# Kernel optimization log

Measured on AMD Instinct MI355X. Metric: run time of the kernel, lower is better.

Reference implementation:

```python
import jax, jax.numpy as jnp
import numpy as np

AXIS = 4  # axis_neuron


def silu(x):
    return x * jax.nn.sigmoid(x)


def setup_inputs() -> dict:
    key = jax.random.key(0)
    ks = jax.random.split(key, 20)
    nf, nloc, nall, nnei, a_sel = 1, 1024, 1024, 64, 20
    n_dim, e_dim, a_dim = 128, 64, 64
    f32 = jnp.float32

    def W(k, i, o):
        return jax.random.normal(k, (i, o), f32) / np.float32(np.sqrt(i))

    angle_in = a_dim + n_dim + 2 * e_dim  # angle_dim with a_compress_rate=0, a_mess_has_n=True
    return {
        "node_ebd_ext": jax.random.normal(ks[0], (nf, nall, n_dim), f32),
        "edge_ebd": jax.random.normal(ks[1], (nf, nloc, nnei, e_dim), f32),
        "h2": jax.random.normal(ks[2], (nf, nloc, nnei, 3), f32),
        "angle_ebd": jax.random.normal(ks[3], (nf, nloc, a_sel, a_sel, a_dim), f32),
        "sw": jax.random.uniform(ks[4], (nf, nloc, nnei), f32),
        "a_sw": jax.random.uniform(ks[5], (nf, nloc, a_sel), f32),
        "W_self": W(ks[6], n_dim, n_dim), "b_self": jnp.zeros((n_dim,), f32),
        "W_sym": W(ks[7], (e_dim + n_dim) * AXIS, n_dim), "b_sym": jnp.zeros((n_dim,), f32),
        "W_ne": W(ks[8], 2 * n_dim + e_dim, n_dim), "b_ne": jnp.zeros((n_dim,), f32),
        "W_es": W(ks[9], 2 * n_dim + e_dim, e_dim), "b_es": jnp.zeros((e_dim,), f32),
        "W_ea1": W(ks[10], angle_in, e_dim), "b_ea1": jnp.zeros((e_dim,), f32),
        "W_ea2": W(ks[11], e_dim, e_dim), "b_ea2": jnp.zeros((e_dim,), f32),
        "W_as": W(ks[12], angle_in, a_dim), "b_as": jnp.zeros((a_dim,), f32),
        "res_n": jnp.full((3, n_dim), 0.1, f32),
        "res_e": jnp.full((2, e_dim), 0.1, f32),
        "res_a": jnp.full((1, a_dim), 0.1, f32),
        "nlist": jax.random.randint(ks[13], (nf, nloc, nnei), 0, nall),
        "nlist_mask": jnp.ones((nf, nloc, nnei), bool),
        "a_nlist_mask": jnp.ones((nf, nloc, a_sel), bool),
    }


def _forward(node_ebd_ext, edge_ebd, h2, angle_ebd, sw, a_sw,
             W_self, b_self, W_sym, b_sym, W_ne, b_ne, W_es, b_es,
             W_ea1, b_ea1, W_ea2, b_ea2, W_as, b_as, res_n, res_e, res_a,
             nlist, nlist_mask, a_nlist_mask):
    nf, nloc, nnei, e_dim = edge_ebd.shape
    a_sel = angle_ebd.shape[2]
    a_dim = angle_ebd.shape[-1]
    n_dim = node_ebd_ext.shape[-1]
    node_ebd = node_ebd_ext[:, :nloc]  # nf x nloc x n_dim

    sw = jnp.where(nlist_mask, sw, 0.0)          # masked switch
    a_sw = jnp.where(a_nlist_mask, a_sw, 0.0)

    # gather neighbor node embeddings: nf x nloc x nnei x n_dim
    idx = jnp.where(nlist_mask, nlist, 0)
    nei_node = jnp.take_along_axis(
        node_ebd_ext, idx.reshape(nf, nloc * nnei)[..., None], axis=1
    ).reshape(nf, nloc, nnei, n_dim)

    # node self mlp
    n_self = silu(node_ebd @ W_self + b_self)

    # symmetrization op: hg = h^T g / nnei; grrg = hg[:axis]^T hg / 3
    def grrg(g):
        gw = g * sw[..., None]
        hg = jnp.einsum('flnt,flnd->fltd', h2, gw) / nnei       # f l 3 d
        out = jnp.einsum('flta,fltd->flad', hg[..., :AXIS], hg) / 3.0
        return out.reshape(nf, nloc, -1)                        # f l (axis*d)

    node_sym = silu(jnp.concatenate([grrg(edge_ebd), grrg(nei_node)], axis=-1) @ W_sym + b_sym)

    # node-edge message: linear over concat([node_i, node_j, edge]) = sum of blocks
    W0, W1, W2 = W_ne[:n_dim], W_ne[n_dim:2 * n_dim], W_ne[2 * n_dim:]
    pre_ne = (node_ebd @ W0)[:, :, None, :] + nei_node @ W1 + edge_ebd @ W2 + b_ne
    n_edge = jnp.sum(silu(pre_ne) * sw[..., None], axis=-2) / nnei

    node_new = node_ebd + res_n[0] * n_self + res_n[1] * node_sym + res_n[2] * n_edge

    # edge self message (same edge_info)
    V0, V1, V2 = W_es[:n_dim], W_es[n_dim:2 * n_dim], W_es[2 * n_dim:]
    edge_self = silu((node_ebd @ V0)[:, :, None, :] + nei_node @ V1 + edge_ebd @ V2 + b_es)

    # ---- angle path ----
    e_ang = jnp.where(a_nlist_mask[..., None], edge_ebd[:, :, :a_sel], 0.0)  # f l a e
    s0, s1, s2 = a_dim, a_dim + n_dim, a_dim + n_dim + e_dim
    A0, A1, A2, A3 = W_ea1[:s0], W_ea1[s0:s1], W_ea1[s1:s2], W_ea1[s2:]
    # angle_info @ W_ea1 without materializing the concat (blocks broadcast)
    pre_ang = (angle_ebd @ A0
               + (node_ebd @ A1)[:, :, None, None, :]
               + (e_ang @ A2)[:, :, None, :, :]   # edge_for_angle_i varies along axis 3
               + (e_ang @ A3)[:, :, :, None, :]   # edge_for_angle_j varies along axis 2
               + b_ea1)
    e_ang_upd = silu(pre_ang)                                     # f l a a e
    weighted = a_sw[:, :, :, None, None] * a_sw[:, :, None, :, None] * e_ang_upd
    reduced = jnp.sum(weighted, axis=-2) / np.float32(np.sqrt(a_sel))  # f l a e
    padded = jnp.pad(reduced, ((0, 0), (0, 0), (0, nnei - a_sel), (0, 0)))
    e_angle_msg = silu(padded @ W_ea2 + b_ea2)
    edge_new = edge_ebd + res_e[0] * edge_self + res_e[1] * e_angle_msg

    # angle self update (same angle_info)
    B0, B1, B2, B3 = W_as[:s0], W_as[s0:s1], W_as[s1:s2], W_as[s2:]
    angle_self = silu(angle_ebd @ B0
                      + (node_ebd @ B1)[:, :, None, None, :]
                      + (e_ang @ B2)[:, :, None, :, :]
                      + (e_ang @ B3)[:, :, :, None, :]
                      + b_as)
    angle_new = angle_ebd + res_a[0] * angle_self
    return node_new, edge_new, angle_new


def reference(node_ebd_ext, edge_ebd, h2, angle_ebd, sw, a_sw,
              W_self, b_self, W_sym, b_sym, W_ne, b_ne, W_es, b_es,
              W_ea1, b_ea1, W_ea2, b_ea2, W_as, b_as, res_n, res_e, res_a,
              nlist, nlist_mask, a_nlist_mask):
    return _forward(node_ebd_ext, edge_ebd, h2, angle_ebd, sw, a_sw,
                    W_self, b_self, W_sym, b_sym, W_ne, b_ne, W_es, b_es,
                    W_ea1, b_ea1, W_ea2, b_ea2, W_as, b_as, res_n, res_e, res_a,
                    nlist, nlist_mask, a_nlist_mask)
```

## Files before the change

### kernel.cpp

```cpp
#include <hip/hip_runtime.h>

#define DEVINL __device__ __forceinline__

#define NLOC 1024
#define NNEI 64
#define NDIM 128
#define EDIM 64
#define ADIM 64
#define ASEL 20

enum : size_t {
  WS_NSELF = 0,
  WS_NW0   = WS_NSELF + 1024*128,
  WS_NV0   = WS_NW0   + 1024*128,
  WS_NA1   = WS_NV0   + 1024*64,
  WS_NB1   = WS_NA1   + 1024*64,
  WS_PA2   = WS_NB1   + 1024*64,
  WS_PA3   = WS_PA2   + 1024*ASEL*64,
  WS_PB2   = WS_PA3   + 1024*ASEL*64,
  WS_PB3   = WS_PB2   + 1024*ASEL*64,
  WS_F32_END = WS_PB3 + 1024*ASEL*64
};
__device__ float g_ws[WS_F32_END];
__device__ float g_red[1024*ASEL*64];

DEVINL float siluf(float x) {
  return x * __builtin_amdgcn_rcpf(1.0f + __expf(-x));
}

__global__ __launch_bounds__(128) void k0_node_pre(
    const float* __restrict__ node,
    const float* __restrict__ W_self, const float* __restrict__ b_self,
    const float* __restrict__ W_ne,   const float* __restrict__ b_ne,
    const float* __restrict__ W_es,   const float* __restrict__ b_es,
    const float* __restrict__ W_ea1,  const float* __restrict__ b_ea1,
    const float* __restrict__ W_as,   const float* __restrict__ b_as)
{
  const int l = blockIdx.x, t = threadIdx.x;
  __shared__ float nl[128];
  nl[t] = node[l*128 + t];
  __syncthreads();
  float aS = b_self[t];
  float aW = b_ne[t];
  #pragma unroll 8
  for (int k = 0; k < 128; ++k) {
    float nv = nl[k];
    aS = fmaf(nv, W_self[k*128 + t], aS);
    aW = fmaf(nv, W_ne[k*128 + t], aW);
  }
  g_ws[WS_NSELF + l*128 + t] = siluf(aS);
  g_ws[WS_NW0   + l*128 + t] = aW;
  if (t < 64) {
    float aV = b_es[t], aA = b_ea1[t], aB = b_as[t];
    #pragma unroll 8
    for (int k = 0; k < 128; ++k) {
      float nv = nl[k];
      aV = fmaf(nv, W_es[k*64 + t], aV);
      aA = fmaf(nv, W_ea1[(64 + k)*64 + t], aA);
      aB = fmaf(nv, W_as[(64 + k)*64 + t], aB);
    }
    g_ws[WS_NV0 + l*64 + t] = aV;
    g_ws[WS_NA1 + l*64 + t] = aA;
    g_ws[WS_NB1 + l*64 + t] = aB;
  }
}

__global__ __launch_bounds__(256) void kp_proj(
    const float* __restrict__ edge,
    const float* __restrict__ W_ea1, const float* __restrict__ W_as)
{
  const int l = blockIdx.x, t = threadIdx.x;
  __shared__ float eang[ASEL*65];
  for (int e = t; e < ASEL*64; e += 256)
    eang[(e >> 6)*65 + (e & 63)] = edge[(size_t)l*4096 + e];
  __syncthreads();
  const int o = t & 63, wv = t >> 6;
  #pragma unroll 1
  for (int m = 0; m < 4; ++m) {
    const float* __restrict__ Wp =
          (m == 0) ? (W_ea1 + 192*64)
        : (m == 1) ? (W_ea1 + 256*64)
        : (m == 2) ? (W_as  + 192*64)
        :            (W_as  + 256*64);
    float* __restrict__ outp = g_ws +
          ((m == 0) ? WS_PA2 : (m == 1) ? WS_PA3 : (m == 2) ? WS_PB2 : WS_PB3)
        + (size_t)l*ASEL*64;
    float a0 = 0.f, a1 = 0.f, a2 = 0.f, a3 = 0.f, a4 = 0.f;
    #pragma unroll 4
    for (int k = 0; k < 64; ++k) {
      float w = Wp[k*64 + o];
      a0 = fmaf(eang[(wv     )*65 + k], w, a0);
      a1 = fmaf(eang[(wv +  4)*65 + k], w, a1);
      a2 = fmaf(eang[(wv +  8)*65 + k], w, a2);
      a3 = fmaf(eang[(wv + 12)*65 + k], w, a3);
      a4 = fmaf(eang[(wv + 16)*65 + k], w, a4);
    }
    outp[(wv     )*64 + o] = a0;
    outp[(wv +  4)*64 + o] = a1;
    outp[(wv +  8)*64 + o] = a2;
    outp[(wv + 12)*64 + o] = a3;
    outp[(wv + 16)*64 + o] = a4;
  }
}

__global__ __launch_bounds__(256, 4) void k2_angle(
    const float* __restrict__ ang,
    const float* __restrict__ a_sw,
    const float* __restrict__ res_a,
    const float* __restrict__ W_ea1, const float* __restrict__ W_as,
    float* __restrict__ angle_out)
{
  const int bid = blockIdx.x;
  const int l = bid / 5, b = bid % 5;
  const int t = threadIdx.x;

  __shared__ __align__(16) float angl[80*68];
  __shared__ __align__(16) float eA2l[ASEL*68], eB2l[ASEL*68];
  __shared__ float aswl[ASEL];

  const float* __restrict__ angbase = ang + ((size_t)l*400 + b*80)*64;
  #pragma unroll
  for (int q = 0; q < 5; ++q) {
    int g = t + q*256;
    int lr = g >> 4, c4 = g & 15;
    float4 v = reinterpret_cast<const float4*>(angbase)[g];
    *reinterpret_cast<float4*>(&angl[lr*68 + c4*4]) = v;
  }
  {
    const float* __restrict__ pa2 = g_ws + WS_PA2 + (size_t)l*ASEL*64;
    const float* __restrict__ pb2 = g_ws + WS_PB2 + (size_t)l*ASEL*64;
    for (int g = t; g < ASEL*16; g += 256) {
      int j = g >> 4, c4 = g & 15;
      *reinterpret_cast<float4*>(&eA2l[j*68 + c4*4]) =
          reinterpret_cast<const float4*>(pa2)[g];
      *reinterpret_cast<float4*>(&eB2l[j*68 + c4*4]) =
          reinterpret_cast<const float4*>(pb2)[g];
    }
  }
  if (t < ASEL) aswl[t] = a_sw[l*ASEL + t];

  const int cg = t & 15, rg = t >> 4;
  const int c0 = cg*4;
  const int i_loc = rg >> 2;
  const int i = b*4 + i_loc;
  const int lr0 = rg*5;

  float4 nA1v = *reinterpret_cast<const float4*>(g_ws + WS_NA1 + l*64 + c0);
  float4 nB1v = *reinterpret_cast<const float4*>(g_ws + WS_NB1 + l*64 + c0);
  float4 eA3v = *reinterpret_cast<const float4*>(g_ws + WS_PA3 + ((size_t)l*ASEL + i)*64 + c0);
  float4 eB3v = *reinterpret_cast<const float4*>(g_ws + WS_PB3 + ((size_t)l*ASEL + i)*64 + c0);
  float4 resav = *reinterpret_cast<const float4*>(res_a + c0);

  __syncthreads();

  const float* __restrict__ A0g = W_ea1;
  const float* __restrict__ B0g = W_as;

  float accA[20], accB[20];
  #pragma unroll
  for (int q = 0; q < 20; ++q) { accA[q] = 0.f; accB[q] = 0.f; }

  #pragma unroll 2
  for (int k = 0; k < 64; k += 4) {
    float vr[5][4];
    #pragma unroll
    for (int q = 0; q < 5; ++q)
      *reinterpret_cast<float4*>(vr[q]) =
          *reinterpret_cast<const float4*>(&angl[(lr0 + q)*68 + k]);
    #pragma unroll
    for (int kk = 0; kk < 4; ++kk) {
      float4 wA = *reinterpret_cast<const float4*>(A0g + (size_t)(k + kk)*64 + c0);
      float4 wB = *reinterpret_cast<const float4*>(B0g + (size_t)(k + kk)*64 + c0);
      #pragma unroll
      for (int q = 0; q < 5; ++q) {
        float av = vr[q][kk];
        accA[q*4+0] = fmaf(av, wA.x, accA[q*4+0]);
        accA[q*4+1] = fmaf(av, wA.y, accA[q*4+1]);
        accA[q*4+2] = fmaf(av, wA.z, accA[q*4+2]);
        accA[q*4+3] = fmaf(av, wA.w, accA[q*4+3]);
        accB[q*4+0] = fmaf(av, wB.x, accB[q*4+0]);
        accB[q*4+1] = fmaf(av, wB.y, accB[q*4+1]);
        accB[q*4+2] = fmaf(av, wB.z, accB[q*4+2]);
        accB[q*4+3] = fmaf(av, wB.w, accB[q*4+3]);
      }
    }
  }

  float red0 = 0.f, red1 = 0.f, red2 = 0.f, red3 = 0.f;
  #pragma unroll
  for (int q = 0; q < 5; ++q) {
    int lr = lr0 + q;
    int j = lr - i_loc*20;
    float aswj = aswl[j];
    float4 e2A = *reinterpret_cast<const float4*>(&eA2l[j*68 + c0]);
    float4 e2B = *reinterpret_cast<const float4*>(&eB2l[j*68 + c0]);
    float4 orig = *reinterpret_cast<const float4*>(&angl[lr*68 + c0]);

    float pA0 = accA[q*4+0] + nA1v.x + e2A.x + eA3v.x;
    float pA1 = accA[q*4+1] + nA1v.y + e2A.y + eA3v.y;
    float pA2 = accA[q*4+2] + nA1v.z + e2A.z + eA3v.z;
    float pA3 = accA[q*4+3] + nA1v.w + e2A.w + eA3v.w;
    red0 = fmaf(aswj, siluf(pA0), red0);
    red1 = fmaf(aswj, siluf(pA1), red1);
    red2 = fmaf(aswj, siluf(pA2), red2);
    red3 = fmaf(aswj, siluf(pA3), red3);

    float pB0 = accB[q*4+0] + nB1v.x + e2B.x + eB3v.x;
    float pB1 = accB[q*4+1] + nB1v.y + e2B.y + eB3v.y;
    float pB2 = accB[q*4+2] + nB1v.z + e2B.z + eB3v.z;
    float pB3 = accB[q*4+3] + nB1v.w + e2B.w + eB3v.w;
    float4 outv;
    outv.x = orig.x + resav.x * siluf(pB0);
    outv.y = orig.y + resav.y * siluf(pB1);
    outv.z = orig.z + resav.z * siluf(pB2);
    outv.w = orig.w + resav.w * siluf(pB3);
    *reinterpret_cast<float4*>(angle_out + ((size_t)l*400 + b*80 + lr)*64 + c0) = outv;
  }

  red0 += __shfl_xor(red0, 16); red0 += __shfl_xor(red0, 32);
  red1 += __shfl_xor(red1, 16); red1 += __shfl_xor(red1, 32);
  red2 += __shfl_xor(red2, 16); red2 += __shfl_xor(red2, 32);
  red3 += __shfl_xor(red3, 16); red3 += __shfl_xor(red3, 32);
  if ((t & 0x30) == 0) {
    float sc = aswl[i] * 0.22360679775f;
    float4 o4 = make_float4(red0*sc, red1*sc, red2*sc, red3*sc);
    *reinterpret_cast<float4*>(g_red + ((size_t)l*ASEL + i)*64 + c0) = o4;
  }
}

__global__ __launch_bounds__(256) void k3_node_edge(
    const float* __restrict__ node_ext,
    const float* __restrict__ edge,
    const float* __restrict__ h2,
    const float* __restrict__ sw,
    const int* __restrict__ nlist,
    const float* __restrict__ W_sym, const float* __restrict__ b_sym,
    const float* __restrict__ W_ne,  const float* __restrict__ W_es,
    const float* __restrict__ W_ea2, const float* __restrict__ b_ea2,
    const float* __restrict__ res_n, const float* __restrict__ res_e,
    float* __restrict__ node_out,
    float* __restrict__ edge_out)
{
  const int l = blockIdx.x, t = threadIdx.x;
  __shared__ float Ef[64*64];
  __shared__ float Nf[64*128];
  __shared__ float hwv[64*4];
  __shared__ float swl[64];
  __shared__ float hgE[3*64], hgN[3*128];
  __shared__ float cat[768];
  __shared__ float nsym[128];
  __shared__ float msgl[ASEL*64];
  __shared__ float msgc[64];

  for (int e = t; e < 4096; e += 256) Ef[e] = edge[l*4096 + e];
  for (int e = t; e < 8192; e += 256) {
    int n = e >> 7, k = e & 127;
    int idx = nlist[l*64 + n];
    Nf[e] = node_ext[(size_t)idx*128 + k];
  }
  if (t < 64) {
    float s = sw[l*64 + t];
    swl[t] = s;
    hwv[t*4+0] = h2[(l*64 + t)*3 + 0] * s;
    hwv[t*4+1] = h2[(l*64 + t)*3 + 1] * s;
    hwv[t*4+2] = h2[(l*64 + t)*3 + 2] * s;
  }
  __syncthreads();

  for (int e = t; e < 192; e += 256) {
    int tt = e >> 6, d = e & 63;
    float acc = 0.f;
    #pragma unroll 4
    for (int n = 0; n < 64; ++n) acc = fmaf(hwv[n*4 + tt], Ef[n*64 + d], acc);
    hgE[tt*64 + d] = acc * (1.f/64.f);
  }
  for (int e = t; e < 384; e += 256) {
    int tt = e >> 7, k = e & 127;
    float acc = 0.f;
    #pragma unroll 4
    for (int n = 0; n < 64; ++n) acc = fmaf(hwv[n*4 + tt], Nf[n*128 + k], acc);
    hgN[tt*128 + k] = acc * (1.f/64.f);
  }
  __syncthreads();

  for (int e = t; e < 256; e += 256) {
    int a = e >> 6, d = e & 63;
    cat[e] = (hgE[a]*hgE[d] + hgE[64 + a]*hgE[64 + d] + hgE[128 + a]*hgE[128 + d]) * (1.f/3.f);
  }
  for (int e = t; e < 512; e += 256) {
    int a = e >> 7, k = e & 127;
    cat[256 + e] = (hgN[a]*hgN[k] + hgN[128 + a]*hgN[128 + k] + hgN[256 + a]*hgN[256 + k]) * (1.f/3.f);
  }
  __syncthreads();

  if (t < 128) {
    float acc = b_sym[t];
    #pragma unroll 4
    for (int c = 0; c < 768; ++c)
      acc = fmaf(cat[c], W_sym[c*128 + t], acc);
    nsym[t] = siluf(acc);
  } else {
    int idx = t - 128;
    if (idx < 64) msgc[idx] = siluf(b_ea2[idx]);
    for (int q = 0; q < 10; ++q) {
      int e = q*128 + idx;
      int n = e >> 6, oo = e & 63;
      float acc = b_ea2[oo];
      #pragma unroll 4
      for (int k = 0; k < 64; ++k)
        acc = fmaf(g_red[(l*ASEL + n)*64 + k], W_ea2[k*64 + oo], acc);
      msgl[e] = siluf(acc);
    }
  }
  __syncthreads();

  if (t < 128) {
    const int c = t;
    float colbase = g_ws[WS_NW0 + l*128 + c];
    float nedge = 0.f;
    for (int nt4 = 0; nt4 < 4; ++nt4) {
      float acc[16];
      #pragma unroll
      for (int nn = 0; nn < 16; ++nn) acc[nn] = colbase;
      #pragma unroll 4
      for (int k = 0; k < 128; ++k) {
        float w = W_ne[(128 + k)*128 + c];
        #pragma unroll
        for (int nn = 0; nn < 16; ++nn)
          acc[nn] = fmaf(Nf[(nt4*16 + nn)*128 + k], w, acc[nn]);
      }
      #pragma unroll 4
      for (int k = 0; k < 64; ++k) {
        float w = W_ne[(256 + k)*128 + c];
        #pragma unroll
        for (int nn = 0; nn < 16; ++nn)
          acc[nn] = fmaf(Ef[(nt4*16 + nn)*64 + k], w, acc[nn]);
      }
      #pragma unroll
      for (int nn = 0; nn < 16; ++nn)
        nedge = fmaf(siluf(acc[nn]), swl[nt4*16 + nn], nedge);
    }
    nedge *= (1.f/64.f);
    float nodev = node_ext[l*128 + c];
    float outv = nodev + res_n[c]*g_ws[WS_NSELF + l*128 + c]
               + res_n[128 + c]*nsym[c] + res_n[256 + c]*nedge;
    node_out[l*128 + c] = outv;
  } else if (t < 192) {
    const int o = t - 128;
    float colbase = g_ws[WS_NV0 + l*64 + o];
    float re0 = res_e[o], re1 = res_e[64 + o];
    float msgcv = msgc[o];
    for (int nt4 = 0; nt4 < 4; ++nt4) {
      float acc[16];
      #pragma unroll
      for (int nn = 0; nn < 16; ++nn) acc[nn] = colbase;
      #pragma unroll 4
      for (int k = 0; k < 128; ++k) {
        float w = W_es[(128 + k)*64 + o];
        #pragma unroll
        for (int nn = 0; nn < 16; ++nn)
          acc[nn] = fmaf(Nf[(nt4*16 + nn)*128 + k], w, acc[nn]);
      }
      #pragma unroll 4
      for (int k = 0; k < 64; ++k) {
        float w = W_es[(256 + k)*64 + o];
        #pragma unroll
        for (int nn = 0; nn < 16; ++nn)
          acc[nn] = fmaf(Ef[(nt4*16 + nn)*64 + k], w, acc[nn]);
      }
      #pragma unroll
      for (int nn = 0; nn < 16; ++nn) {
        int n = nt4*16 + nn;
        float s = siluf(acc[nn]);
        float msgv = (n < ASEL) ? msgl[n*64 + o] : msgcv;
        edge_out[(size_t)l*4096 + n*64 + o] = Ef[n*64 + o] + re0*s + re1*msgv;
      }
    }
  }
}

extern "C" void kernel_launch(void* const* d_in, const int* in_sizes, int n_in,
                              void* d_out, int out_size, void* d_ws, size_t ws_size,
                              hipStream_t stream) {
  const float* node_ext = (const float*)d_in[0];
  const float* edge_ebd = (const float*)d_in[1];
  const float* h2       = (const float*)d_in[2];
  const float* angle    = (const float*)d_in[3];
  const float* sw       = (const float*)d_in[4];
  const float* a_sw     = (const float*)d_in[5];
  const float* W_self   = (const float*)d_in[6];
  const float* b_self   = (const float*)d_in[7];
  const float* W_sym    = (const float*)d_in[8];
  const float* b_sym    = (const float*)d_in[9];
  const float* W_ne     = (const float*)d_in[10];
  const float* b_ne     = (const float*)d_in[11];
  const float* W_es     = (const float*)d_in[12];
  const float* b_es     = (const float*)d_in[13];
  const float* W_ea1    = (const float*)d_in[14];
  const float* b_ea1    = (const float*)d_in[15];
  const float* W_ea2    = (const float*)d_in[16];
  const float* b_ea2    = (const float*)d_in[17];
  const float* W_as     = (const float*)d_in[18];
  const float* b_as     = (const float*)d_in[19];
  const float* res_n    = (const float*)d_in[20];
  const float* res_e    = (const float*)d_in[21];
  const float* res_a    = (const float*)d_in[22];
  const int*   nlist    = (const int*)d_in[23];

  float* out = (float*)d_out;
  float* node_out  = out;
  float* edge_out  = out + 1024*128;
  float* angle_out = out + 1024*128 + (size_t)1024*64*64;

  k0_node_pre<<<1024, 128, 0, stream>>>(node_ext, W_self, b_self, W_ne, b_ne,
                                        W_es, b_es, W_ea1, b_ea1, W_as, b_as);
  kp_proj<<<1024, 256, 0, stream>>>(edge_ebd, W_ea1, W_as);
  k2_angle<<<1024*5, 256, 0, stream>>>(angle, a_sw, res_a,
                                       W_ea1, W_as, angle_out);
  k3_node_edge<<<1024, 256, 0, stream>>>(node_ext, edge_ebd, h2, sw, nlist,
                                         W_sym, b_sym, W_ne, W_es, W_ea2, b_ea2,
                                         res_n, res_e, node_out, edge_out);
}
```

Baseline: 686.1 us.

## Retile k3 node/edge GEMM across all threads with register blocking and staged weights

The per-neighbor node/edge matmuls in k3 previously ran on only 192 of 256 threads, each streaming weights from global memory. They now run as a register-blocked 64x192 tile GEMM over all threads: a 4x12 output tile per thread, with K-chunks of W_ne and W_es staged through shared memory and prefetched into registers. Neighbor gathers use float4 loads into a padded combined buffer. The node reduction over neighbors uses shuffles plus shared atomics. This adds register pressure (launch bounds set to 2 blocks per CU) and more syncs per K-chunk.

```diff
diff --git a/kernel.cpp b/kernel.cpp
--- a/kernel.cpp
+++ b/kernel.cpp
@@ -228,7 +228,7 @@
   }
 }
 
-__global__ __launch_bounds__(256) void k3_node_edge(
+__global__ __launch_bounds__(256, 2) void k3_node_edge(
     const float* __restrict__ node_ext,
     const float* __restrict__ edge,
     const float* __restrict__ h2,
@@ -242,8 +242,8 @@
     float* __restrict__ edge_out)
 {
   const int l = blockIdx.x, t = threadIdx.x;
-  __shared__ float Ef[64*64];
-  __shared__ float Nf[64*128];
+  __shared__ __align__(16) float AL[64*196];
+  __shared__ __align__(16) float WL[16*192];
   __shared__ float hwv[64*4];
   __shared__ float swl[64];
   __shared__ float hgE[3*64], hgN[3*128];
@@ -251,13 +251,11 @@
   __shared__ float nsym[128];
   __shared__ float msgl[ASEL*64];
   __shared__ float msgc[64];
-
-  for (int e = t; e < 4096; e += 256) Ef[e] = edge[l*4096 + e];
-  for (int e = t; e < 8192; e += 256) {
-    int n = e >> 7, k = e & 127;
-    int idx = nlist[l*64 + n];
-    Nf[e] = node_ext[(size_t)idx*128 + k];
-  }
+  __shared__ float redn[128];
+  __shared__ int   idxl[64];
+
+  if (t < 64) idxl[t] = nlist[l*64 + t];
+  if (t >= 64 && t < 192) redn[t - 64] = 0.f;
   if (t < 64) {
     float s = sw[l*64 + t];
     swl[t] = s;
@@ -267,18 +265,30 @@
   }
   __syncthreads();
 
+  for (int g = t; g < 2048; g += 256) {
+    int n = g >> 5, q = g & 31;
+    float4 v = *reinterpret_cast<const float4*>(node_ext + (size_t)idxl[n]*128 + q*4);
+    *reinterpret_cast<float4*>(&AL[n*196 + q*4]) = v;
+  }
+  for (int g = t; g < 1024; g += 256) {
+    int n = g >> 4, q = g & 15;
+    float4 v = *reinterpret_cast<const float4*>(edge + (size_t)l*4096 + n*64 + q*4);
+    *reinterpret_cast<float4*>(&AL[n*196 + 128 + q*4]) = v;
+  }
+  __syncthreads();
+
   for (int e = t; e < 192; e += 256) {
     int tt = e >> 6, d = e & 63;
     float acc = 0.f;
     #pragma unroll 4
-    for (int n = 0; n < 64; ++n) acc = fmaf(hwv[n*4 + tt], Ef[n*64 + d], acc);
+    for (int n = 0; n < 64; ++n) acc = fmaf(hwv[n*4 + tt], AL[n*196 + 128 + d], acc);
     hgE[tt*64 + d] = acc * (1.f/64.f);
   }
   for (int e = t; e < 384; e += 256) {
     int tt = e >> 7, k = e & 127;
     float acc = 0.f;
     #pragma unroll 4
-    for (int n = 0; n < 64; ++n) acc = fmaf(hwv[n*4 + tt], Nf[n*128 + k], acc);
+    for (int n = 0; n < 64; ++n) acc = fmaf(hwv[n*4 + tt], AL[n*196 + k], acc);
     hgN[tt*128 + k] = acc * (1.f/64.f);
   }
   __syncthreads();
@@ -308,74 +318,137 @@
       float acc = b_ea2[oo];
       #pragma unroll 4
       for (int k = 0; k < 64; ++k)
-        acc = fmaf(g_red[(l*ASEL + n)*64 + k], W_ea2[k*64 + oo], acc);
+        acc = fmaf(g_red[((size_t)l*ASEL + n)*64 + k], W_ea2[k*64 + oo], acc);
       msgl[e] = siluf(acc);
+    }
+  }
+
+  const int tx = t & 15, ty = t >> 4;
+  const int n0 = ty*4, c0 = tx*12;
+
+  float acc[4][12];
+  #pragma unroll
+  for (int r = 0; r < 4; ++r)
+    #pragma unroll
+    for (int cc = 0; cc < 12; ++cc) acc[r][cc] = 0.f;
+
+  float4 wreg[3];
+  #pragma unroll
+  for (int q = 0; q < 3; ++q) {
+    int g = q*256 + t;
+    int kk = g / 48, c4 = g % 48;
+    int c = c4*4, krow = 128 + kk;
+    wreg[q] = (c < 128)
+        ? *reinterpret_cast<const float4*>(W_ne + (size_t)krow*128 + c)
+        : *reinterpret_cast<const float4*>(W_es + (size_t)krow*64 + (c - 128));
+  }
+
+  #pragma unroll 1
+  for (int kb = 0; kb < 12; ++kb) {
+    __syncthreads();
+    #pragma unroll
+    for (int q = 0; q < 3; ++q) {
+      int g = q*256 + t;
+      int kk = g / 48, c4 = g % 48;
+      *reinterpret_cast<float4*>(&WL[kk*192 + c4*4]) = wreg[q];
+    }
+    if (kb < 11) {
+      #pragma unroll
+      for (int q = 0; q < 3; ++q) {
+        int g = q*256 + t;
+        int kk = g / 48, c4 = g % 48;
+        int c = c4*4, krow = 128 + (kb + 1)*16 + kk;
+        wreg[q] = (c < 128)
+            ? *reinterpret_cast<const float4*>(W_ne + (size_t)krow*128 + c)
+            : *reinterpret_cast<const float4*>(W_es + (size_t)krow*64 + (c - 128));
+      }
+    }
+    __syncthreads();
+
+    const int kbase = kb*16;
+    #pragma unroll
+    for (int kk = 0; kk < 16; kk += 4) {
+      float ar[4][4];
+      #pragma unroll
+      for (int r = 0; r < 4; ++r)
+        *reinterpret_cast<float4*>(ar[r]) =
+            *reinterpret_cast<const float4*>(&AL[(n0 + r)*196 + kbase + kk]);
+      #pragma unroll
+      for (int j = 0; j < 4; ++j) {
+        float4 w0 = *reinterpret_cast<const float4*>(&WL[(kk + j)*192 + c0]);
+        float4 w1 = *reinterpret_cast<const float4*>(&WL[(kk + j)*192 + c0 + 4]);
+        float4 w2 = *reinterpret_cast<const float4*>(&WL[(kk + j)*192 + c0 + 8]);
+        #pragma unroll
+        for (int r = 0; r < 4; ++r) {
+          float av = ar[r][j];
+          acc[r][0]  = fmaf(av, w0.x, acc[r][0]);
+          acc[r][1]  = fmaf(av, w0.y, acc[r][1]);
+          acc[r][2]  = fmaf(av, w0.z, acc[r][2]);
+          acc[r][3]  = fmaf(av, w0.w, acc[r][3]);
+          acc[r][4]  = fmaf(av, w1.x, acc[r][4]);
+          acc[r][5]  = fmaf(av, w1.y, acc[r][5]);
+          acc[r][6]  = fmaf(av, w1.z, acc[r][6]);
+          acc[r][7]  = fmaf(av, w1.w, acc[r][7]);
+          acc[r][8]  = fmaf(av, w2.x, acc[r][8]);
+          acc[r][9]  = fmaf(av, w2.y, acc[r][9]);
+          acc[r][10] = fmaf(av, w2.z, acc[r][10]);
+          acc[r][11] = fmaf(av, w2.w, acc[r][11]);
+        }
+      }
+    }
+  }
+
+  float colb[12];
+  #pragma unroll
+  for (int cc = 0; cc < 12; ++cc) {
+    int c = c0 + cc;
+    colb[cc] = (c < 128) ? g_ws[WS_NW0 + l*128 + c]
+                         : g_ws[WS_NV0 + l*64 + (c - 128)];
+  }
+  float np[12];
+  #pragma unroll
+  for (int cc = 0; cc < 12; ++cc) np[cc] = 0.f;
+
+  #pragma unroll
+  for (int r = 0; r < 4; ++r) {
+    int n = n0 + r;
+    float sn = swl[n];
+    #pragma unroll
+    for (int cc = 0; cc < 12; ++cc) {
+      int c = c0 + cc;
+      float s = siluf(acc[r][cc] + colb[cc]);
+      if (c < 128) {
+        np[cc] = fmaf(s, sn, np[cc]);
+      } else {
+        int o = c - 128;
+        float msgv = (n < ASEL) ? msgl[n*64 + o] : msgc[o];
+        float ef = AL[n*196 + 128 + o];
+        edge_out[(size_t)l*4096 + n*64 + o] =
+            ef + res_e[o]*s + res_e[64 + o]*msgv;
+      }
+    }
+  }
+
+  #pragma unroll
+  for (int cc = 0; cc < 12; ++cc) {
+    np[cc] += __shfl_xor(np[cc], 16);
+    np[cc] += __shfl_xor(np[cc], 32);
+  }
+  if ((ty & 3) == 0) {
+    #pragma unroll
+    for (int cc = 0; cc < 12; ++cc) {
+      int c = c0 + cc;
+      if (c < 128) atomicAdd(&redn[c], np[cc]);
     }
   }
   __syncthreads();
 
   if (t < 128) {
     const int c = t;
-    float colbase = g_ws[WS_NW0 + l*128 + c];
-    float nedge = 0.f;
-    for (int nt4 = 0; nt4 < 4; ++nt4) {
-      float acc[16];
-      #pragma unroll
-      for (int nn = 0; nn < 16; ++nn) acc[nn] = colbase;
-      #pragma unroll 4
-      for (int k = 0; k < 128; ++k) {
-        float w = W_ne[(128 + k)*128 + c];
-        #pragma unroll
-        for (int nn = 0; nn < 16; ++nn)
-          acc[nn] = fmaf(Nf[(nt4*16 + nn)*128 + k], w, acc[nn]);
-      }
-      #pragma unroll 4
-      for (int k = 0; k < 64; ++k) {
-        float w = W_ne[(256 + k)*128 + c];
-        #pragma unroll
-        for (int nn = 0; nn < 16; ++nn)
-          acc[nn] = fmaf(Ef[(nt4*16 + nn)*64 + k], w, acc[nn]);
-      }
-      #pragma unroll
-      for (int nn = 0; nn < 16; ++nn)
-        nedge = fmaf(siluf(acc[nn]), swl[nt4*16 + nn], nedge);
-    }
-    nedge *= (1.f/64.f);
+    float nedge = redn[c] * (1.f/64.f);
     float nodev = node_ext[l*128 + c];
-    float outv = nodev + res_n[c]*g_ws[WS_NSELF + l*128 + c]
-               + res_n[128 + c]*nsym[c] + res_n[256 + c]*nedge;
-    node_out[l*128 + c] = outv;
-  } else if (t < 192) {
-    const int o = t - 128;
-    float colbase = g_ws[WS_NV0 + l*64 + o];
-    float re0 = res_e[o], re1 = res_e[64 + o];
-    float msgcv = msgc[o];
-    for (int nt4 = 0; nt4 < 4; ++nt4) {
-      float acc[16];
-      #pragma unroll
-      for (int nn = 0; nn < 16; ++nn) acc[nn] = colbase;
-      #pragma unroll 4
-      for (int k = 0; k < 128; ++k) {
-        float w = W_es[(128 + k)*64 + o];
-        #pragma unroll
-        for (int nn = 0; nn < 16; ++nn)
-          acc[nn] = fmaf(Nf[(nt4*16 + nn)*128 + k], w, acc[nn]);
-      }
-      #pragma unroll 4
-      for (int k = 0; k < 64; ++k) {
-        float w = W_es[(256 + k)*64 + o];
-        #pragma unroll
-        for (int nn = 0; nn < 16; ++nn)
-          acc[nn] = fmaf(Ef[(nt4*16 + nn)*64 + k], w, acc[nn]);
-      }
-      #pragma unroll
-      for (int nn = 0; nn < 16; ++nn) {
-        int n = nt4*16 + nn;
-        float s = siluf(acc[nn]);
-        float msgv = (n < ASEL) ? msgl[n*64 + o] : msgcv;
-        edge_out[(size_t)l*4096 + n*64 + o] = Ef[n*64 + o] + re0*s + re1*msgv;
-      }
-    }
+    node_out[l*128 + c] = nodev + res_n[c]*g_ws[WS_NSELF + l*128 + c]
+                        + res_n[128 + c]*nsym[c] + res_n[256 + c]*nedge;
   }
 }
 
```

After: 653.0 us. 4.8% less time.
